# Kernel tuning notes

Measured on AMD Instinct MI355X. Metric: run time of the kernel, lower is better.

## Reference

```python
import jax, jax.numpy as jnp
import numpy as np

N = 50000      # nodes
E = 800000     # edges
F = 128        # num_node_features
H = 128        # hidden_dim
DEPTH = 4
G = 512        # number of graphs in batch
BN_EPS = 1e-5


def setup_inputs() -> dict:
    key = jax.random.key(0)
    ks = jax.random.split(key, 10)
    x = jax.random.normal(ks[0], (N, F), dtype=jnp.float32)
    edge_index = jax.random.randint(ks[1], (2, E), 0, N, dtype=jnp.int64)
    batch = jnp.sort(jax.random.randint(ks[2], (N,), 0, G, dtype=jnp.int64))
    W_emb = jax.random.normal(ks[3], (F, H), dtype=jnp.float32) / np.sqrt(F)
    b_emb = jnp.zeros((H,), dtype=jnp.float32)
    W_conv = jax.random.normal(ks[4], (DEPTH, H, H), dtype=jnp.float32) / np.sqrt(H)
    b_conv = jnp.zeros((DEPTH, H), dtype=jnp.float32)
    gamma = jnp.ones((DEPTH - 1, H), dtype=jnp.float32)
    beta = jnp.zeros((DEPTH - 1, H), dtype=jnp.float32)
    return {"x": x, "edge_index": edge_index, "batch": batch,
            "W_emb": W_emb, "b_emb": b_emb, "W_conv": W_conv,
            "b_conv": b_conv, "gamma": gamma, "beta": beta}


def _gcn_conv(h, W, b, src, dst, dinv):
    # PyG GCNConv: D^{-1/2}(A+I)D^{-1/2} (h W) + b, with self-loops folded in
    hw = h @ W  # [N, H]
    norm = dinv[src] * dinv[dst]  # [E]
    agg = jax.ops.segment_sum(norm[:, None] * hw[src], dst, num_segments=N)
    agg = agg + (dinv * dinv)[:, None] * hw  # self-loop contribution
    return agg + b


def _batchnorm(h, g, b):
    mu = jnp.mean(h, axis=0)
    var = jnp.var(h, axis=0)
    return (h - mu) * jax.lax.rsqrt(var + BN_EPS) * g + b


def reference(x, edge_index, batch, W_emb, b_emb, W_conv, b_conv, gamma, beta):
    src, dst = edge_index[0], edge_index[1]
    # degrees incl. self-loop for symmetric GCN normalization
    deg = jax.ops.segment_sum(jnp.ones((E,), jnp.float32), dst, num_segments=N) + 1.0
    dinv = jax.lax.rsqrt(deg)
    h = x @ W_emb + b_emb  # embedding Linear
    for i in range(DEPTH):
        h = _gcn_conv(h, W_conv[i], b_conv[i], src, dst, dinv)
        if i < DEPTH - 1:
            h = jax.nn.relu(h)
            h = _batchnorm(h, gamma[i], beta[i])
    # global mean pool over graph ids
    counts = jax.ops.segment_sum(jnp.ones((N,), jnp.float32), batch, num_segments=G)
    pooled = jax.ops.segment_sum(h, batch, num_segments=G)
    return pooled / jnp.maximum(counts, 1.0)[:, None]
```

## Files before the change

### kernel.cpp

```cpp
#include <hip/hip_runtime.h>
#include <hip/hip_fp16.h>
#include <math.h>

#define HDIM 128
#define BKT_SHIFT 7
#define NBMAX 512
#define CHUNK 4096

typedef __attribute__((ext_vector_type(8))) short bf16x8;
typedef __attribute__((ext_vector_type(4))) float f32x4;

union U4 { unsigned int u[4]; bf16x8 v; };

__device__ __forceinline__ unsigned int cvt_pk_bf16(float a, float b) {
    unsigned int r;
    asm("v_cvt_pk_bf16_f32 %0, %1, %2" : "=v"(r) : "v"(a), "v"(b));
    return r;
}

__device__ __forceinline__ void split8(const float* v, bf16x8& ah, bf16x8& al) {
    U4 H, L;
    #pragma unroll
    for (int p = 0; p < 4; p++) {
        unsigned int h = cvt_pk_bf16(v[2 * p], v[2 * p + 1]);
        H.u[p] = h;
        float h0 = __uint_as_float(h << 16);
        float h1 = __uint_as_float(h & 0xFFFF0000u);
        L.u[p] = cvt_pk_bf16(v[2 * p] - h0, v[2 * p + 1] - h1);
    }
    ah = H.v; al = L.v;
}

__global__ __launch_bounds__(256) void bucket_hist(const int* __restrict__ dst,
                                                   int* __restrict__ bcount, int E) {
    __shared__ int h[NBMAX];
    int t = threadIdx.x;
    for (int b = t; b < NBMAX; b += 256) h[b] = 0;
    __syncthreads();
    int i = blockIdx.x * blockDim.x + t;
    int stride = gridDim.x * blockDim.x;
    for (; i < E; i += stride) atomicAdd(&h[dst[i] >> BKT_SHIFT], 1);
    __syncthreads();
    for (int b = t; b < NBMAX; b += 256) {
        int c = h[b];
        if (c) atomicAdd(&bcount[b], c);
    }
}

__global__ __launch_bounds__(256) void bucket_scan(const int* __restrict__ bcount,
                                                   int* __restrict__ bases,
                                                   int* __restrict__ cursor, int E) {
    int t = threadIdx.x;
    int v0 = bcount[2 * t], v1 = bcount[2 * t + 1];
    int s = v0 + v1;
    __shared__ int ss[256];
    ss[t] = s; __syncthreads();
    #pragma unroll
    for (int off = 1; off < 256; off <<= 1) {
        int u = (t >= off) ? ss[t - off] : 0;
        __syncthreads();
        ss[t] += u;
        __syncthreads();
    }
    int ex = ss[t] - s;
    bases[2 * t] = ex;          cursor[2 * t] = ex;
    bases[2 * t + 1] = ex + v0; cursor[2 * t + 1] = ex + v0;
    if (t == 255) bases[NBMAX] = E;
}

__global__ __launch_bounds__(256) void bucket_scatter(const int* __restrict__ src,
                                                      const int* __restrict__ dst,
                                                      int* __restrict__ cursor,
                                                      unsigned* __restrict__ ebuf, int E) {
    __shared__ unsigned sbuf[CHUNK];
    __shared__ int hist[NBMAX], hbase[NBMAX], gbase[NBMAX], cnt2[NBMAX];
    __shared__ int ss[256];
    int t = threadIdx.x;
    int start = blockIdx.x * CHUNK;
    int n = min(CHUNK, E - start);

    for (int b = t; b < NBMAX; b += 256) { hist[b] = 0; cnt2[b] = 0; }
    __syncthreads();
    for (int i = t; i < n; i += 256) atomicAdd(&hist[dst[start + i] >> BKT_SHIFT], 1);
    __syncthreads();

    int v0 = hist[2 * t], v1 = hist[2 * t + 1];
    int s = v0 + v1;
    ss[t] = s; __syncthreads();
    #pragma unroll
    for (int off = 1; off < 256; off <<= 1) {
        int u = (t >= off) ? ss[t - off] : 0;
        __syncthreads();
        ss[t] += u;
        __syncthreads();
    }
    int ex = ss[t] - s;
    hbase[2 * t] = ex;
    hbase[2 * t + 1] = ex + v0;
    if (v0 > 0) gbase[2 * t] = atomicAdd(&cursor[2 * t], v0);
    if (v1 > 0) gbase[2 * t + 1] = atomicAdd(&cursor[2 * t + 1], v1);
    __syncthreads();

    for (int i = t; i < n; i += 256) {
        int d = dst[start + i];
        int bkt = d >> BKT_SHIFT;
        unsigned p = ((unsigned)(d & 127) << 24) | (unsigned)src[start + i];
        int pos = atomicAdd(&cnt2[bkt], 1);
        sbuf[hbase[bkt] + pos] = p;
    }
    __syncthreads();

    for (int b = t; b < NBMAX; b += 256) {
        int c = hist[b], hb = hbase[b], gb = gbase[b];
        for (int j = 0; j < c; j++) ebuf[gb + j] = sbuf[hb + j];
    }
}

__global__ __launch_bounds__(256) void bucket_finalize(const unsigned* __restrict__ ebuf,
                                                       const int* __restrict__ bases,
                                                       int* __restrict__ csr,
                                                       int* __restrict__ offs,
                                                       float* __restrict__ dinv,
                                                       int N, int E) {
    int b = blockIdx.x;
    int beg = bases[b], end = bases[b + 1];
    __shared__ int hist[128], pre[128], cnt2[128];
    int t = threadIdx.x;
    if (t < 128) { hist[t] = 0; cnt2[t] = 0; }
    __syncthreads();
    for (int i = beg + t; i < end; i += 256)
        atomicAdd(&hist[(ebuf[i] >> 24) & 127], 1);
    __syncthreads();
    if (t < 128) pre[t] = hist[t];
    __syncthreads();
    #pragma unroll
    for (int off = 1; off < 128; off <<= 1) {
        int v = (t < 128 && t >= off) ? pre[t - off] : 0;
        __syncthreads();
        if (t < 128) pre[t] += v;
        __syncthreads();
    }
    if (t < 128) {
        int node = b * 128 + t;
        if (node < N) {
            int ex = pre[t] - hist[t];
            offs[node] = beg + ex;
            dinv[node] = rsqrtf((float)hist[t] + 1.0f);
        }
    }
    if (b == 0 && t == 0) offs[N] = E;
    __syncthreads();
    for (int i = beg + t; i < end; i += 256) {
        unsigned p = ebuf[i];
        int dl = (p >> 24) & 127;
        int pos = atomicAdd(&cnt2[dl], 1);
        csr[beg + (pre[dl] - hist[dl]) + pos] = (int)(p & 0xFFFFFFu);
    }
}

__global__ void wsplit_all(const float* __restrict__ W_emb, const float* __restrict__ W_conv,
                           short* __restrict__ wt) {
    int gid = blockIdx.x * 256 + threadIdx.x;
    if (gid >= 5 * 16384) return;
    int m = gid >> 14;
    int i = gid & 16383;
    int n = i >> 7, k = i & 127;
    const float* src = (m == 0) ? W_emb : (W_conv + (size_t)(m - 1) * 16384);
    float v = src[k * 128 + n];
    unsigned int u = __float_as_uint(v);
    unsigned int hi = (u + 0x7FFFu + ((u >> 16) & 1)) & 0xFFFF0000u;
    float hf = __uint_as_float(hi);
    float lo = v - hf;
    unsigned int ul = __float_as_uint(lo);
    unsigned int lo16 = (ul + 0x7FFFu + ((ul >> 16) & 1)) >> 16;
    short* Whi = wt + (size_t)m * 32768;
    Whi[i] = (short)(hi >> 16);
    Whi[16384 + i] = (short)lo16;
}

template <bool OUT_F16>
__global__ __launch_bounds__(256) void gemm_mfma(const float* __restrict__ A,
                                                 const short* __restrict__ Wh,
                                                 const short* __restrict__ Wl,
                                                 const float* __restrict__ aff_s,
                                                 const float* __restrict__ aff_t,
                                                 const float* __restrict__ bias,
                                                 const float* __restrict__ rowscale,
                                                 void* __restrict__ outp, int N) {
    int w = threadIdx.x >> 6;
    int lane = threadIdx.x & 63;
    int l15 = lane & 15, lg = lane >> 4;
    int r0 = blockIdx.x * 128 + (w >> 1) * 64;
    int c0 = (w & 1) * 64;

    f32x4 acc[4][4];
    #pragma unroll
    for (int tc = 0; tc < 4; tc++) {
        float bz = bias ? bias[c0 + tc * 16 + l15] : 0.0f;
        #pragma unroll
        for (int tr = 0; tr < 4; tr++) {
            acc[tr][tc][0] = bz; acc[tr][tc][1] = bz;
            acc[tr][tc][2] = bz; acc[tr][tc][3] = bz;
        }
    }

    #pragma unroll
    for (int kt = 0; kt < 4; kt++) {
        int kk = kt * 32 + lg * 8;

        bf16x8 bh[4], bl[4];
        #pragma unroll
        for (int tc = 0; tc < 4; tc++) {
            int n = c0 + tc * 16 + l15;
            bh[tc] = *(const bf16x8*)(Wh + n * 128 + kk);
            bl[tc] = *(const bf16x8*)(Wl + n * 128 + kk);
        }

        float sv[8], tv[8];
        if (aff_s) {
            *(float4*)&sv[0] = *(const float4*)(aff_s + kk);
            *(float4*)&sv[4] = *(const float4*)(aff_s + kk + 4);
            *(float4*)&tv[0] = *(const float4*)(aff_t + kk);
            *(float4*)&tv[4] = *(const float4*)(aff_t + kk + 4);
        }

        bf16x8 ah[4], al[4];
        #pragma unroll
        for (int tr = 0; tr < 4; tr++) {
            int row = min(r0 + tr * 16 + l15, N - 1);
            const float* ap = A + (size_t)row * 128 + kk;
            float v[8];
            *(float4*)&v[0] = *(const float4*)ap;
            *(float4*)&v[4] = *(const float4*)(ap + 4);
            if (aff_s) {
                #pragma unroll
                for (int j = 0; j < 8; j++) v[j] = fmaf(v[j], sv[j], tv[j]);
            }
            split8(v, ah[tr], al[tr]);
        }

        #pragma unroll
        for (int tr = 0; tr < 4; tr++) {
            #pragma unroll
            for (int tc = 0; tc < 4; tc++) {
                acc[tr][tc] = __builtin_amdgcn_mfma_f32_16x16x32_bf16(ah[tr], bh[tc], acc[tr][tc], 0, 0, 0);
                acc[tr][tc] = __builtin_amdgcn_mfma_f32_16x16x32_bf16(ah[tr], bl[tc], acc[tr][tc], 0, 0, 0);
                acc[tr][tc] = __builtin_amdgcn_mfma_f32_16x16x32_bf16(al[tr], bh[tc], acc[tr][tc], 0, 0, 0);
            }
        }
    }

    #pragma unroll
    for (int tr = 0; tr < 4; tr++) {
        #pragma unroll
        for (int r = 0; r < 4; r++) {
            int row = r0 + tr * 16 + lg * 4 + r;
            if (row < N) {
                float sc = rowscale ? rowscale[row] : 1.0f;
                #pragma unroll
                for (int tc = 0; tc < 4; tc++) {
                    int col = c0 + tc * 16 + l15;
                    float val = acc[tr][tc][r] * sc;
                    if (OUT_F16) {
                        ((__half*)outp)[(size_t)row * 128 + col] = __float2half(val);
                    } else {
                        ((float*)outp)[(size_t)row * 128 + col] = val;
                    }
                }
            }
        }
    }
}

__global__ __launch_bounds__(256) void gather_kernel(const __half* __restrict__ hws,
                                                     const int* __restrict__ csr_src,
                                                     const int* __restrict__ offs,
                                                     const float* __restrict__ dinv,
                                                     const float* __restrict__ bias,
                                                     float* __restrict__ out,
                                                     int N, int relu) {
    int lane = threadIdx.x & 63;
    int half = lane >> 5;
    int sl = lane & 31;
    int node = blockIdx.x * 4 + (threadIdx.x >> 6);
    if (node >= N) return;
    int lo = offs[node], hi = offs[node + 1];

    const uint2* base = (const uint2*)hws;
    float4 acc = make_float4(0.f, 0.f, 0.f, 0.f);

    int j = lo + half;
    for (; j + 6 < hi; j += 8) {
        int s0 = csr_src[j], s1 = csr_src[j + 2], s2 = csr_src[j + 4], s3 = csr_src[j + 6];
        uint2 u0 = base[(size_t)s0 * 32 + sl];
        uint2 u1 = base[(size_t)s1 * 32 + sl];
        uint2 u2 = base[(size_t)s2 * 32 + sl];
        uint2 u3 = base[(size_t)s3 * 32 + sl];
        float2 a0 = __half22float2(*(__half2*)&u0.x), b0 = __half22float2(*(__half2*)&u0.y);
        float2 a1 = __half22float2(*(__half2*)&u1.x), b1 = __half22float2(*(__half2*)&u1.y);
        float2 a2 = __half22float2(*(__half2*)&u2.x), b2 = __half22float2(*(__half2*)&u2.y);
        float2 a3 = __half22float2(*(__half2*)&u3.x), b3 = __half22float2(*(__half2*)&u3.y);
        acc.x += a0.x + a1.x + a2.x + a3.x;
        acc.y += a0.y + a1.y + a2.y + a3.y;
        acc.z += b0.x + b1.x + b2.x + b3.x;
        acc.w += b0.y + b1.y + b2.y + b3.y;
    }
    for (; j < hi; j += 2) {
        int s = csr_src[j];
        uint2 u = base[(size_t)s * 32 + sl];
        float2 a = __half22float2(*(__half2*)&u.x), b = __half22float2(*(__half2*)&u.y);
        acc.x += a.x; acc.y += a.y; acc.z += b.x; acc.w += b.y;
    }
    if (half == 0) {
        uint2 u = base[(size_t)node * 32 + sl];
        float2 a = __half22float2(*(__half2*)&u.x), b = __half22float2(*(__half2*)&u.y);
        acc.x += a.x; acc.y += a.y; acc.z += b.x; acc.w += b.y;
    }
    acc.x += __shfl_xor(acc.x, 32);
    acc.y += __shfl_xor(acc.y, 32);
    acc.z += __shfl_xor(acc.z, 32);
    acc.w += __shfl_xor(acc.w, 32);

    if (half == 0) {
        float di = dinv[node];
        float4 b = ((const float4*)bias)[sl];
        float ox = di * acc.x + b.x;
        float oy = di * acc.y + b.y;
        float oz = di * acc.z + b.z;
        float ow = di * acc.w + b.w;
        if (relu) {
            ox = fmaxf(ox, 0.f); oy = fmaxf(oy, 0.f);
            oz = fmaxf(oz, 0.f); ow = fmaxf(ow, 0.f);
        }
        ((float4*)(out + (size_t)node * HDIM))[sl] = make_float4(ox, oy, oz, ow);
    }
}

__global__ __launch_bounds__(256) void bn_stats_kernel(const float* __restrict__ h,
                                                       float* __restrict__ stats, int N) {
    int f = threadIdx.x & 127;
    int half_ = threadIdx.x >> 7;
    float s = 0.f, s2 = 0.f;
    for (int n = blockIdx.x * 2 + half_; n < N; n += gridDim.x * 2) {
        float v = h[(size_t)n * HDIM + f];
        s += v;
        s2 += v * v;
    }
    __shared__ float ls[256], ls2[256];
    ls[threadIdx.x] = s;
    ls2[threadIdx.x] = s2;
    __syncthreads();
    if (half_ == 0) {
        s = ls[f] + ls[f + 128];
        s2 = ls2[f] + ls2[f + 128];
        atomicAdd(&stats[f], s);
        atomicAdd(&stats[128 + f], s2);
    }
}

__global__ void bn_finalize(const float* __restrict__ stats, const float* __restrict__ gamma,
                            const float* __restrict__ beta, float* __restrict__ aff_s,
                            float* __restrict__ aff_t, int N) {
    int f = threadIdx.x;
    float inv = 1.0f / (float)N;
    float m = stats[f] * inv;
    float var = stats[128 + f] * inv - m * m;
    float s = gamma[f] * rsqrtf(var + 1e-5f);
    aff_s[f] = s;
    aff_t[f] = beta[f] - m * s;
}

__device__ __forceinline__ int lower_bound_i(const int* __restrict__ arr, int n, int val) {
    int lo = 0, hi = n;
    while (lo < hi) {
        int mid = (lo + hi) >> 1;
        if (arr[mid] < val) lo = mid + 1; else hi = mid;
    }
    return lo;
}

__global__ __launch_bounds__(256) void pool_kernel(const float* __restrict__ h,
                                                   const int* __restrict__ batch,
                                                   float* __restrict__ out, int N, int G) {
    int g = blockIdx.x;
    int lo = lower_bound_i(batch, N, g);
    int hi = lower_bound_i(batch, N, g + 1);
    int sl = threadIdx.x & 31;
    int rg = threadIdx.x >> 5;

    float4 acc = make_float4(0.f, 0.f, 0.f, 0.f);
    for (int n = lo + rg; n < hi; n += 8) {
        float4 v = ((const float4*)(h + (size_t)n * HDIM))[sl];
        acc.x += v.x; acc.y += v.y; acc.z += v.z; acc.w += v.w;
    }

    __shared__ float4 red[256];
    red[threadIdx.x] = acc;
    __syncthreads();
    if (rg < 4) {
        float4 o = red[threadIdx.x + 128];
        acc.x += o.x; acc.y += o.y; acc.z += o.z; acc.w += o.w;
        red[threadIdx.x] = acc;
    }
    __syncthreads();
    if (rg < 2) {
        float4 o = red[threadIdx.x + 64];
        acc.x += o.x; acc.y += o.y; acc.z += o.z; acc.w += o.w;
        red[threadIdx.x] = acc;
    }
    __syncthreads();
    if (rg == 0) {
        float4 o = red[threadIdx.x + 32];
        float inv = 1.0f / fmaxf((float)(hi - lo), 1.0f);
        float4 r;
        r.x = (acc.x + o.x) * inv;
        r.y = (acc.y + o.y) * inv;
        r.z = (acc.z + o.z) * inv;
        r.w = (acc.w + o.w) * inv;
        ((float4*)(out + (size_t)g * HDIM))[sl] = r;
    }
}

extern "C" void kernel_launch(void* const* d_in, const int* in_sizes, int n_in,
                              void* d_out, int out_size, void* d_ws, size_t ws_size,
                              hipStream_t stream) {
    const float* x      = (const float*)d_in[0];
    const int*   ei     = (const int*)d_in[1];
    const int*   batch  = (const int*)d_in[2];
    const float* W_emb  = (const float*)d_in[3];
    const float* b_emb  = (const float*)d_in[4];
    const float* W_conv = (const float*)d_in[5];
    const float* b_conv = (const float*)d_in[6];
    const float* gamma  = (const float*)d_in[7];
    const float* beta   = (const float*)d_in[8];

    const int E = in_sizes[1] / 2;
    const int N = in_sizes[2];
    const int G = out_size / HDIM;
    const int DEPTH = 4;

    const int* srcp = ei;
    const int* dstp = ei + E;
    float* out = (float*)d_out;

    size_t NH = (size_t)N * HDIM;
    size_t npad = ((size_t)N + 63) & ~(size_t)63;
    size_t epad = ((size_t)E + 63) & ~(size_t)63;
    int nb = (N + 127) / 128;

    float* ws = (float*)d_ws;
    float* dinv    = ws;
    int*   offs    = (int*)(dinv + npad);
    int*   bases   = offs + npad + 64;
    int*   cursor  = bases + 1024;
    int*   bcount  = cursor + NBMAX;
    int*   csr     = bcount + NBMAX;
    unsigned* ebuf = (unsigned*)(csr + epad);
    float* stats   = (float*)(ebuf + epad);
    float* aff_s   = stats + 256;
    float* aff_t   = aff_s + 128;
    short* wt      = (short*)(aff_t + 128);
    float* hbuf    = (float*)(wt + 5 * 2 * 16384);
    __half* hws16  = (__half*)(hbuf + NH);

    wsplit_all<<<(5 * 16384 + 255) / 256, 256, 0, stream>>>(W_emb, W_conv, wt);

    hipMemsetAsync(bcount, 0, NBMAX * sizeof(int), stream);
    bucket_hist<<<256, 256, 0, stream>>>(dstp, bcount, E);
    bucket_scan<<<1, 256, 0, stream>>>(bcount, bases, cursor, E);
    bucket_scatter<<<(E + CHUNK - 1) / CHUNK, 256, 0, stream>>>(srcp, dstp, cursor, ebuf, E);
    bucket_finalize<<<nb, 256, 0, stream>>>(ebuf, bases, csr, offs, dinv, N, E);

    int gemm_blocks = (N + 127) / 128;

    gemm_mfma<false><<<gemm_blocks, 256, 0, stream>>>(x, wt, wt + 16384, nullptr, nullptr,
                                                      b_emb, nullptr, hbuf, N);

    int gather_blocks = (N + 3) / 4;

    for (int l = 0; l < DEPTH; l++) {
        short* whi = wt + (size_t)(l + 1) * 32768;
        gemm_mfma<true><<<gemm_blocks, 256, 0, stream>>>(hbuf, whi, whi + 16384,
                                                         (l > 0) ? aff_s : nullptr,
                                                         (l > 0) ? aff_t : nullptr,
                                                         nullptr, dinv, hws16, N);
        gather_kernel<<<gather_blocks, 256, 0, stream>>>(hws16, csr, offs, dinv,
                                                         b_conv + (size_t)l * HDIM, hbuf,
                                                         N, (l < DEPTH - 1) ? 1 : 0);
        if (l < DEPTH - 1) {
            hipMemsetAsync(stats, 0, 256 * sizeof(float), stream);
            bn_stats_kernel<<<512, 256, 0, stream>>>(hbuf, stats, N);
            bn_finalize<<<1, 128, 0, stream>>>(stats, gamma + (size_t)l * HDIM,
                                               beta + (size_t)l * HDIM, aff_s, aff_t, N);
        }
    }

    pool_kernel<<<G, 256, 0, stream>>>(hbuf, batch, out, N, G);
}
```

Measured before the change: 403.6 us.

## Fold BatchNorm affine into next-layer weights and store activations as split bf16

The per-feature BatchNorm scale is folded into the next layer's weight matrix, which a new small kernel re-splits into bf16 hi/lo. The shift becomes a bias vector t·W, computed in the finalize kernel. Activations are now stored directly as bf16 hi/lo planes by the gather kernel, so the GEMM loads ready-made MFMA operands and skips the per-element affine and float-to-bf16 split. This costs an extra weight-split launch and a serial 128-term dot product per layer, and the folded weights carry slightly different rounding.

```diff
diff --git a/kernel.cpp b/kernel.cpp
--- a/kernel.cpp
+++ b/kernel.cpp
@@ -178,15 +178,30 @@
     Whi[16384 + i] = (short)lo16;
 }
 
-template <bool OUT_F16>
-__global__ __launch_bounds__(256) void gemm_mfma(const float* __restrict__ A,
+__global__ void wsplit_scaled(const float* __restrict__ Wsrc, const float* __restrict__ aff_s,
+                              short* __restrict__ Whi) {
+    int i = blockIdx.x * 256 + threadIdx.x;
+    if (i >= 16384) return;
+    int n = i >> 7, k = i & 127;
+    float v = Wsrc[k * 128 + n] * aff_s[k];
+    unsigned int u = __float_as_uint(v);
+    unsigned int hi = (u + 0x7FFFu + ((u >> 16) & 1)) & 0xFFFF0000u;
+    float hf = __uint_as_float(hi);
+    float lo = v - hf;
+    unsigned int ul = __float_as_uint(lo);
+    unsigned int lo16 = (ul + 0x7FFFu + ((ul >> 16) & 1)) >> 16;
+    Whi[i] = (short)(hi >> 16);
+    Whi[16384 + i] = (short)lo16;
+}
+
+template <bool IN_SPLIT, bool OUT_SPLIT>
+__global__ __launch_bounds__(256) void gemm_mfma(const void* __restrict__ Ap,
                                                  const short* __restrict__ Wh,
                                                  const short* __restrict__ Wl,
-                                                 const float* __restrict__ aff_s,
-                                                 const float* __restrict__ aff_t,
                                                  const float* __restrict__ bias,
                                                  const float* __restrict__ rowscale,
-                                                 void* __restrict__ outp, int N) {
+                                                 void* __restrict__ outp,
+                                                 size_t NH, int N) {
     int w = threadIdx.x >> 6;
     int lane = threadIdx.x & 63;
     int l15 = lane & 15, lg = lane >> 4;
@@ -216,27 +231,21 @@
             bl[tc] = *(const bf16x8*)(Wl + n * 128 + kk);
         }
 
-        float sv[8], tv[8];
-        if (aff_s) {
-            *(float4*)&sv[0] = *(const float4*)(aff_s + kk);
-            *(float4*)&sv[4] = *(const float4*)(aff_s + kk + 4);
-            *(float4*)&tv[0] = *(const float4*)(aff_t + kk);
-            *(float4*)&tv[4] = *(const float4*)(aff_t + kk + 4);
-        }
-
         bf16x8 ah[4], al[4];
         #pragma unroll
         for (int tr = 0; tr < 4; tr++) {
             int row = min(r0 + tr * 16 + l15, N - 1);
-            const float* ap = A + (size_t)row * 128 + kk;
-            float v[8];
-            *(float4*)&v[0] = *(const float4*)ap;
-            *(float4*)&v[4] = *(const float4*)(ap + 4);
-            if (aff_s) {
-                #pragma unroll
-                for (int j = 0; j < 8; j++) v[j] = fmaf(v[j], sv[j], tv[j]);
+            if (IN_SPLIT) {
+                const short* Ahi = (const short*)Ap;
+                ah[tr] = *(const bf16x8*)(Ahi + (size_t)row * 128 + kk);
+                al[tr] = *(const bf16x8*)(Ahi + NH + (size_t)row * 128 + kk);
+            } else {
+                const float* ap = (const float*)Ap + (size_t)row * 128 + kk;
+                float v[8];
+                *(float4*)&v[0] = *(const float4*)ap;
+                *(float4*)&v[4] = *(const float4*)(ap + 4);
+                split8(v, ah[tr], al[tr]);
             }
-            split8(v, ah[tr], al[tr]);
         }
 
         #pragma unroll
@@ -261,10 +270,17 @@
                 for (int tc = 0; tc < 4; tc++) {
                     int col = c0 + tc * 16 + l15;
                     float val = acc[tr][tc][r] * sc;
-                    if (OUT_F16) {
+                    if (OUT_SPLIT) {
+                        unsigned int u = __float_as_uint(val);
+                        unsigned int hi = (u + 0x7FFFu + ((u >> 16) & 1)) & 0xFFFF0000u;
+                        float lof = val - __uint_as_float(hi);
+                        unsigned int ul = __float_as_uint(lof);
+                        unsigned int lo16 = (ul + 0x7FFFu + ((ul >> 16) & 1)) >> 16;
+                        short* Ohi = (short*)outp;
+                        Ohi[(size_t)row * 128 + col] = (short)(hi >> 16);
+                        Ohi[NH + (size_t)row * 128 + col] = (short)lo16;
+                    } else {
                         ((__half*)outp)[(size_t)row * 128 + col] = __float2half(val);
-                    } else {
-                        ((float*)outp)[(size_t)row * 128 + col] = val;
                     }
                 }
             }
@@ -272,13 +288,14 @@
     }
 }
 
+template <bool OUT_SPLIT>
 __global__ __launch_bounds__(256) void gather_kernel(const __half* __restrict__ hws,
                                                      const int* __restrict__ csr_src,
                                                      const int* __restrict__ offs,
                                                      const float* __restrict__ dinv,
                                                      const float* __restrict__ bias,
-                                                     float* __restrict__ out,
-                                                     int N, int relu) {
+                                                     void* __restrict__ outp,
+                                                     size_t NH, int N) {
     int lane = threadIdx.x & 63;
     int half = lane >> 5;
     int sl = lane & 31;
@@ -328,46 +345,80 @@
         float oy = di * acc.y + b.y;
         float oz = di * acc.z + b.z;
         float ow = di * acc.w + b.w;
-        if (relu) {
+        if (OUT_SPLIT) {
             ox = fmaxf(ox, 0.f); oy = fmaxf(oy, 0.f);
             oz = fmaxf(oz, 0.f); ow = fmaxf(ow, 0.f);
-        }
-        ((float4*)(out + (size_t)node * HDIM))[sl] = make_float4(ox, oy, oz, ow);
-    }
-}
-
-__global__ __launch_bounds__(256) void bn_stats_kernel(const float* __restrict__ h,
-                                                       float* __restrict__ stats, int N) {
-    int f = threadIdx.x & 127;
-    int half_ = threadIdx.x >> 7;
-    float s = 0.f, s2 = 0.f;
-    for (int n = blockIdx.x * 2 + half_; n < N; n += gridDim.x * 2) {
-        float v = h[(size_t)n * HDIM + f];
-        s += v;
-        s2 += v * v;
-    }
-    __shared__ float ls[256], ls2[256];
-    ls[threadIdx.x] = s;
-    ls2[threadIdx.x] = s2;
-    __syncthreads();
-    if (half_ == 0) {
-        s = ls[f] + ls[f + 128];
-        s2 = ls2[f] + ls2[f + 128];
-        atomicAdd(&stats[f], s);
-        atomicAdd(&stats[128 + f], s2);
-    }
-}
-
-__global__ void bn_finalize(const float* __restrict__ stats, const float* __restrict__ gamma,
-                            const float* __restrict__ beta, float* __restrict__ aff_s,
-                            float* __restrict__ aff_t, int N) {
+            unsigned h0 = cvt_pk_bf16(ox, oy), h1 = cvt_pk_bf16(oz, ow);
+            float hx = __uint_as_float(h0 << 16), hy = __uint_as_float(h0 & 0xFFFF0000u);
+            float hz = __uint_as_float(h1 << 16), hw = __uint_as_float(h1 & 0xFFFF0000u);
+            unsigned l0 = cvt_pk_bf16(ox - hx, oy - hy), l1 = cvt_pk_bf16(oz - hz, ow - hw);
+            short* Ohi = (short*)outp;
+            ((uint2*)(Ohi + (size_t)node * 128))[sl] = make_uint2(h0, h1);
+            ((uint2*)(Ohi + NH + (size_t)node * 128))[sl] = make_uint2(l0, l1);
+        } else {
+            ((float4*)((float*)outp + (size_t)node * HDIM))[sl] = make_float4(ox, oy, oz, ow);
+        }
+    }
+}
+
+__global__ __launch_bounds__(256) void bn_stats2(const short* __restrict__ Ahi,
+                                                 float* __restrict__ stats,
+                                                 size_t NH, int N) {
+    int sl = threadIdx.x & 31;
+    int rg = threadIdx.x >> 5;
+    const short* Alo = Ahi + NH;
+    float4 s = make_float4(0.f, 0.f, 0.f, 0.f), q = s;
+    for (int n = blockIdx.x * 8 + rg; n < N; n += gridDim.x * 8) {
+        uint2 uh = ((const uint2*)(Ahi + (size_t)n * 128))[sl];
+        uint2 ul = ((const uint2*)(Alo + (size_t)n * 128))[sl];
+        float vx = __uint_as_float(uh.x << 16) + __uint_as_float(ul.x << 16);
+        float vy = __uint_as_float(uh.x & 0xFFFF0000u) + __uint_as_float(ul.x & 0xFFFF0000u);
+        float vz = __uint_as_float(uh.y << 16) + __uint_as_float(ul.y << 16);
+        float vw = __uint_as_float(uh.y & 0xFFFF0000u) + __uint_as_float(ul.y & 0xFFFF0000u);
+        s.x += vx; q.x += vx * vx;
+        s.y += vy; q.y += vy * vy;
+        s.z += vz; q.z += vz * vz;
+        s.w += vw; q.w += vw * vw;
+    }
+    __shared__ float4 rs[256], rq[256];
+    rs[threadIdx.x] = s; rq[threadIdx.x] = q;
+    __syncthreads();
+    #pragma unroll
+    for (int off = 4; off >= 1; off >>= 1) {
+        if (rg < off) {
+            float4 os = rs[threadIdx.x + off * 32], oq = rq[threadIdx.x + off * 32];
+            s.x += os.x; s.y += os.y; s.z += os.z; s.w += os.w;
+            q.x += oq.x; q.y += oq.y; q.z += oq.z; q.w += oq.w;
+            rs[threadIdx.x] = s; rq[threadIdx.x] = q;
+        }
+        __syncthreads();
+    }
+    if (rg == 0) {
+        atomicAdd(&stats[4 * sl + 0], s.x); atomicAdd(&stats[4 * sl + 1], s.y);
+        atomicAdd(&stats[4 * sl + 2], s.z); atomicAdd(&stats[4 * sl + 3], s.w);
+        atomicAdd(&stats[128 + 4 * sl + 0], q.x); atomicAdd(&stats[128 + 4 * sl + 1], q.y);
+        atomicAdd(&stats[128 + 4 * sl + 2], q.z); atomicAdd(&stats[128 + 4 * sl + 3], q.w);
+    }
+}
+
+__global__ void bn_finalize_w(const float* __restrict__ stats, const float* __restrict__ gamma,
+                              const float* __restrict__ beta, const float* __restrict__ Wnext,
+                              float* __restrict__ aff_s, float* __restrict__ aff_t,
+                              float* __restrict__ cvec, int N) {
     int f = threadIdx.x;
     float inv = 1.0f / (float)N;
     float m = stats[f] * inv;
     float var = stats[128 + f] * inv - m * m;
     float s = gamma[f] * rsqrtf(var + 1e-5f);
+    float t_ = beta[f] - m * s;
     aff_s[f] = s;
-    aff_t[f] = beta[f] - m * s;
+    aff_t[f] = t_;
+    __shared__ float ts[128];
+    ts[f] = t_;
+    __syncthreads();
+    float c = 0.f;
+    for (int k = 0; k < 128; k++) c += ts[k] * Wnext[k * 128 + f];
+    cvec[f] = c;
 }
 
 __device__ __forceinline__ int lower_bound_i(const int* __restrict__ arr, int n, int val) {
@@ -459,9 +510,11 @@
     float* stats   = (float*)(ebuf + epad);
     float* aff_s   = stats + 256;
     float* aff_t   = aff_s + 128;
-    short* wt      = (short*)(aff_t + 128);
+    float* cvec    = aff_t + 128;
+    short* wt      = (short*)(cvec + 128);
     float* hbuf    = (float*)(wt + 5 * 2 * 16384);
     __half* hws16  = (__half*)(hbuf + NH);
+    short* hsplit  = (short*)hbuf;
 
     wsplit_all<<<(5 * 16384 + 255) / 256, 256, 0, stream>>>(W_emb, W_conv, wt);
 
@@ -472,26 +525,31 @@
     bucket_finalize<<<nb, 256, 0, stream>>>(ebuf, bases, csr, offs, dinv, N, E);
 
     int gemm_blocks = (N + 127) / 128;
-
-    gemm_mfma<false><<<gemm_blocks, 256, 0, stream>>>(x, wt, wt + 16384, nullptr, nullptr,
-                                                      b_emb, nullptr, hbuf, N);
-
     int gather_blocks = (N + 3) / 4;
+
+    gemm_mfma<false, true><<<gemm_blocks, 256, 0, stream>>>(x, wt, wt + 16384, b_emb,
+                                                            nullptr, hsplit, NH, N);
 
     for (int l = 0; l < DEPTH; l++) {
         short* whi = wt + (size_t)(l + 1) * 32768;
-        gemm_mfma<true><<<gemm_blocks, 256, 0, stream>>>(hbuf, whi, whi + 16384,
-                                                         (l > 0) ? aff_s : nullptr,
-                                                         (l > 0) ? aff_t : nullptr,
-                                                         nullptr, dinv, hws16, N);
-        gather_kernel<<<gather_blocks, 256, 0, stream>>>(hws16, csr, offs, dinv,
-                                                         b_conv + (size_t)l * HDIM, hbuf,
-                                                         N, (l < DEPTH - 1) ? 1 : 0);
+        gemm_mfma<true, false><<<gemm_blocks, 256, 0, stream>>>(hsplit, whi, whi + 16384,
+                                                                (l > 0) ? cvec : nullptr,
+                                                                dinv, hws16, NH, N);
         if (l < DEPTH - 1) {
+            gather_kernel<true><<<gather_blocks, 256, 0, stream>>>(hws16, csr, offs, dinv,
+                                                                   b_conv + (size_t)l * HDIM,
+                                                                   hsplit, NH, N);
             hipMemsetAsync(stats, 0, 256 * sizeof(float), stream);
-            bn_stats_kernel<<<512, 256, 0, stream>>>(hbuf, stats, N);
-            bn_finalize<<<1, 128, 0, stream>>>(stats, gamma + (size_t)l * HDIM,
-                                               beta + (size_t)l * HDIM, aff_s, aff_t, N);
+            bn_stats2<<<512, 256, 0, stream>>>(hsplit, stats, NH, N);
+            const float* Wnext = W_conv + (size_t)(l + 1) * 16384;
+            bn_finalize_w<<<1, 128, 0, stream>>>(stats, gamma + (size_t)l * HDIM,
+                                                 beta + (size_t)l * HDIM, Wnext,
+                                                 aff_s, aff_t, cvec, N);
+            wsplit_scaled<<<64, 256, 0, stream>>>(Wnext, aff_s, wt + (size_t)(l + 2) * 32768);
+        } else {
+            gather_kernel<false><<<gather_blocks, 256, 0, stream>>>(hws16, csr, offs, dinv,
+                                                                    b_conv + (size_t)l * HDIM,
+                                                                    hbuf, NH, N);
         }
     }
 
```

Result: slower. 505.6 us (+25.3%).
